# Optimization experiments

Measured on AMD Instinct MI355X. Metric: run time of the kernel, lower is better.

Reference implementation:

```python
import jax, jax.numpy as jnp
import numpy as np
from jax import lax

T, IN, H, OUT = 8192, 1, 1024, 1


def setup_inputs() -> dict:
    key = jax.random.key(0)
    ks = jax.random.split(key, 7)
    s = 1.0 / np.sqrt(H)
    return {
        "x": jax.random.normal(ks[0], (T, IN), dtype=jnp.float32),
        "W_ih": jax.random.uniform(ks[1], (4 * H, IN), jnp.float32, -s, s),
        "W_hh": jax.random.uniform(ks[2], (4 * H, H), jnp.float32, -s, s),
        "b_ih": jax.random.uniform(ks[3], (4 * H,), jnp.float32, -s, s),
        "b_hh": jax.random.uniform(ks[4], (4 * H,), jnp.float32, -s, s),
        "W_fc": jax.random.uniform(ks[5], (OUT, H), jnp.float32, -s, s),
        "b_fc": jax.random.uniform(ks[6], (OUT,), jnp.float32, -s, s),
    }


def reference(x, W_ih, W_hh, b_ih, b_hh, W_fc, b_fc):
    # x: (T, input_size); batch dim of 1 is squeezed out.
    H_ = W_hh.shape[1]
    # Precompute input contribution to all gates for every timestep: (T, 4H)
    xg = x @ W_ih.T + (b_ih + b_hh)

    def step(carry, gx):
        h, c = carry
        g = gx + h @ W_hh.T  # (4H,) -- PyTorch gate order i, f, g, o
        i, f, gg, o = jnp.split(g, 4)
        c = jax.nn.sigmoid(f) * c + jax.nn.sigmoid(i) * jnp.tanh(gg)
        h = jax.nn.sigmoid(o) * jnp.tanh(c)
        return (h, c), h

    h0 = jnp.zeros((H_,), dtype=x.dtype)
    c0 = jnp.zeros((H_,), dtype=x.dtype)
    _, hs = lax.scan(step, (h0, c0), xg)  # hs: (T, H)
    return hs @ W_fc.T + b_fc  # (T, output_size)
```

## Files before the change

### kernel.cpp

```cpp
#include <hip/hip_runtime.h>

#define TT    8192
#define HD    1024
#define NBLK  256
#define NTHR  256
#define NBUF  4
#define NREP  8

typedef int i32x4 __attribute__((ext_vector_type(4)));
typedef int i32x2 __attribute__((ext_vector_type(2)));

__device__ __forceinline__ void llc_load_pair(const unsigned* p, i32x4& a, i32x4& b) {
  asm volatile("global_load_dwordx4 %0, %2, off sc0 sc1\n\t"
               "global_load_dwordx4 %1, %3, off sc0 sc1\n\t"
               "s_waitcnt vmcnt(0)"
               : "=&v"(a), "=&v"(b)
               : "v"(p), "v"(p + 4)
               : "memory");
}
__device__ __forceinline__ unsigned llc_load1(const unsigned* p) {
  unsigned r;
  asm volatile("global_load_dword %0, %1, off sc0 sc1\n\ts_waitcnt vmcnt(0)"
               : "=v"(r) : "v"(p) : "memory");
  return r;
}
__device__ __forceinline__ void llc_store2(unsigned* p, unsigned lo, unsigned hi) {
  i32x2 v; v.x = (int)lo; v.y = (int)hi;
  asm volatile("global_store_dwordx2 %0, %1, off sc0 sc1"
               :: "v"(p), "v"(v) : "memory");
}
__device__ __forceinline__ void llc_store1(unsigned* p, unsigned v) {
  asm volatile("global_store_dword %0, %1, off sc0 sc1"
               :: "v"(p), "v"(v) : "memory");
}

__device__ __forceinline__ float sigf(float z) {
  return 1.0f / (1.0f + __expf(-z));
}
__device__ __forceinline__ float tanh_fast(float z) {
  float az = fabsf(z);
  float e  = __expf(2.0f * az);
  float t  = 1.0f - 2.0f / (e + 1.0f);
  return z < 0.0f ? -t : t;
}

#define FMA4(acc, hvv, wvv)                                      \
  acc = fmaf((hvv).x, (wvv).x, acc);                             \
  acc = fmaf((hvv).y, (wvv).y, acc);                             \
  acc = fmaf((hvv).z, (wvv).z, acc);                             \
  acc = fmaf((hvv).w, (wvv).w, acc);

extern "C" __global__ __launch_bounds__(NTHR, 1)
void lstm_persistent(const float* __restrict__ x,
                     const float* __restrict__ W_ih,
                     const float* __restrict__ W_hh,
                     const float* __restrict__ b_ih,
                     const float* __restrict__ b_hh,
                     const float* __restrict__ W_fc,
                     const float* __restrict__ b_fc,
                     float* __restrict__ out,
                     unsigned* __restrict__ flag,
                     unsigned* __restrict__ hbuf)
{
  const int tid = threadIdx.x;
  const int blk = blockIdx.x;

  if (blk == NBLK) {
    for (int t = 0; t < TT; ++t) {
      const unsigned* src = hbuf + (((t & (NBUF - 1)) * HD + tid * 4) * 2);
      i32x4 A, B;
      const int want = t + 1;
      do {
        llc_load_pair(src, A, B);
      } while (!(A.y == want && A.w == want && B.y == want && B.w == want));
      __syncthreads();
      if (tid < NREP)
        llc_store1(flag + (tid << 4), (unsigned)want);
    }
    return;
  }

  __shared__ float x_lds[TT];
  __shared__ float h_lds[HD];

  const int wave = tid >> 6;
  const int lane = tid & 63;
  const int g    = lane >> 4;
  const int kc   = lane & 15;
  const int unit = blk * 4 + wave;

  for (int i = tid; i < TT / 4; i += NTHR)
    ((float4*)x_lds)[i] = ((const float4*)x)[i];

  float4 w4[16];
  {
    const float* wr = W_hh + (size_t)(g * HD + unit) * HD + kc * 4;
#pragma unroll
    for (int m = 0; m < 16; ++m)
      w4[m] = *((const float4*)(wr + m * 64));
  }
  float4 wfc4[4];
#pragma unroll
  for (int m = 0; m < 4; ++m)
    wfc4[m] = *((const float4*)(W_fc + m * 256 + lane * 4));
  const float bfc_val = b_fc[0];

  float wih_g[4], bs_g[4];
#pragma unroll
  for (int q = 0; q < 4; ++q) {
    int r = q * HD + unit;
    wih_g[q] = W_ih[r];
    bs_g[q]  = b_ih[r] + b_hh[r];
  }
  float c_state = 0.0f;
  __syncthreads();

  const unsigned* flag_mine = flag + ((blk & (NREP - 1)) << 4);

  for (int t = 0; t < TT; ++t) {
    const bool doproj = (t > 0) && (wave == 1) && (blk == (t & 255));
    float accs = 0.0f;
    float4 hp4[4];

    if (t > 0) {
      while (llc_load1(flag_mine) < (unsigned)t) { }
      const unsigned* src = hbuf + (((t - 1) & (NBUF - 1)) * HD + tid * 4) * 2;
      i32x4 A, B;
      llc_load_pair(src, A, B);
      float4 hv;
      hv.x = __int_as_float(A.x); hv.y = __int_as_float(A.z);
      hv.z = __int_as_float(B.x); hv.w = __int_as_float(B.z);
      ((float4*)h_lds)[tid] = hv;
      __syncthreads();

      const float* hp = h_lds + kc * 4;
      float s0 = 0.f, s1 = 0.f, s2 = 0.f, s3 = 0.f;
#pragma unroll
      for (int mb = 0; mb < 4; ++mb) {
        float4 ha = *((const float4*)(hp + (mb * 4 + 0) * 64));
        float4 hb = *((const float4*)(hp + (mb * 4 + 1) * 64));
        float4 hc = *((const float4*)(hp + (mb * 4 + 2) * 64));
        float4 hd = *((const float4*)(hp + (mb * 4 + 3) * 64));
        FMA4(s0, ha, w4[mb * 4 + 0]);
        FMA4(s1, hb, w4[mb * 4 + 1]);
        FMA4(s2, hc, w4[mb * 4 + 2]);
        FMA4(s3, hd, w4[mb * 4 + 3]);
      }
      accs = (s0 + s1) + (s2 + s3);

      if (doproj) {
#pragma unroll
        for (int m = 0; m < 4; ++m)
          hp4[m] = *((const float4*)(h_lds + m * 256 + lane * 4));
      }
    }

#pragma unroll
    for (int s = 1; s < 16; s <<= 1)
      accs += __shfl_xor(accs, s);

    float gi = __shfl(accs, 0);
    float gf = __shfl(accs, 16);
    float gg = __shfl(accs, 32);
    float go = __shfl(accs, 48);

    if (lane == 0) {
      float xt = x_lds[t];
      gi += fmaf(xt, wih_g[0], bs_g[0]);
      gf += fmaf(xt, wih_g[1], bs_g[1]);
      gg += fmaf(xt, wih_g[2], bs_g[2]);
      go += fmaf(xt, wih_g[3], bs_g[3]);
      c_state  = sigf(gf) * c_state + sigf(gi) * tanh_fast(gg);
      float hn = sigf(go) * tanh_fast(c_state);
      llc_store2(hbuf + (((t & (NBUF - 1)) * HD + unit) * 2),
                 __float_as_uint(hn), (unsigned)(t + 1));
    }

    if (doproj) {
      float p = 0.f;
#pragma unroll
      for (int m = 0; m < 4; ++m) { FMA4(p, hp4[m], wfc4[m]); }
#pragma unroll
      for (int s = 1; s < 64; s <<= 1) p += __shfl_xor(p, s);
      if (lane == 0) out[t - 1] = p + bfc_val;
    }
  }

  if (blk == 0) {
    const unsigned* src = hbuf + (((TT - 1) & (NBUF - 1)) * HD + tid * 4) * 2;
    i32x4 A, B;
    do {
      llc_load_pair(src, A, B);
    } while (!(A.y == TT && A.w == TT && B.y == TT && B.w == TT));
    float4 hv;
    hv.x = __int_as_float(A.x); hv.y = __int_as_float(A.z);
    hv.z = __int_as_float(B.x); hv.w = __int_as_float(B.z);
    ((float4*)h_lds)[tid] = hv;
    __syncthreads();
    if (wave == 1) {
      float p = 0.f;
#pragma unroll
      for (int m = 0; m < 4; ++m) {
        float4 hm = *((const float4*)(h_lds + m * 256 + lane * 4));
        FMA4(p, hm, wfc4[m]);
      }
#pragma unroll
      for (int s = 1; s < 64; s <<= 1) p += __shfl_xor(p, s);
      if (lane == 0) out[TT - 1] = p + bfc_val;
    }
  }
}

extern "C" void kernel_launch(void* const* d_in, const int* in_sizes, int n_in,
                              void* d_out, int out_size, void* d_ws, size_t ws_size,
                              hipStream_t stream) {
  const float* x   = (const float*)d_in[0];
  const float* Wih = (const float*)d_in[1];
  const float* Whh = (const float*)d_in[2];
  const float* bih = (const float*)d_in[3];
  const float* bhh = (const float*)d_in[4];
  const float* Wfc = (const float*)d_in[5];
  const float* bfc = (const float*)d_in[6];
  float* out = (float*)d_out;

  unsigned* flag = (unsigned*)d_ws;
  unsigned* hbuf = flag + NREP * 16;
  size_t init_bytes = (NREP * 16 + NBUF * HD * 2) * sizeof(unsigned);

  hipMemsetAsync(d_ws, 0, init_bytes, stream);
  hipLaunchKernelGGL(lstm_persistent, dim3(NBLK + 1), dim3(NTHR), 0, stream,
                     x, Wih, Whh, bih, bhh, Wfc, bfc, out, flag, hbuf);
}
```

Baseline: 23.68 ms.

## Relay hidden state through per-XCD L2 mirror to cut cross-die polling latency

In each XCD, the first block to claim a slot through an atomic becomes a relay. Each step, the relay polls the LLC-coherent hidden-state buffer and copies it into a per-XCD mirror. The other blocks on that XCD poll the mirror with L2-scoped loads, aiming to avoid the round trip to LLC and the central flag. A bounded retry count falls back to the original flag path if the mirror stalls. The risks are plain non-coherent stores and L2 visibility ordering, plus the extra relay latency added to the critical path.

```diff
diff --git a/kernel.cpp b/kernel.cpp
--- a/kernel.cpp
+++ b/kernel.cpp
@@ -6,6 +6,8 @@
 #define NTHR  256
 #define NBUF  4
 #define NREP  8
+#define NXCD  8
+#define L2_TRIES 64
 
 typedef int i32x4 __attribute__((ext_vector_type(4)));
 typedef int i32x2 __attribute__((ext_vector_type(2)));
@@ -31,6 +33,18 @@
 }
 __device__ __forceinline__ void llc_store1(unsigned* p, unsigned v) {
   asm volatile("global_store_dword %0, %1, off sc0 sc1"
+               :: "v"(p), "v"(v) : "memory");
+}
+__device__ __forceinline__ void l2_load_pair(const unsigned* p, i32x4& a, i32x4& b) {
+  asm volatile("global_load_dwordx4 %0, %2, off sc0\n\t"
+               "global_load_dwordx4 %1, %3, off sc0\n\t"
+               "s_waitcnt vmcnt(0)"
+               : "=&v"(a), "=&v"(b)
+               : "v"(p), "v"(p + 4)
+               : "memory");
+}
+__device__ __forceinline__ void l2_store4(unsigned* p, i32x4 v) {
+  asm volatile("global_store_dwordx4 %0, %1, off"
                :: "v"(p), "v"(v) : "memory");
 }
 
@@ -59,8 +73,10 @@
                      const float* __restrict__ W_fc,
                      const float* __restrict__ b_fc,
                      float* __restrict__ out,
+                     int*      __restrict__ relay_slot,
                      unsigned* __restrict__ flag,
-                     unsigned* __restrict__ hbuf)
+                     unsigned* __restrict__ hbuf,
+                     unsigned* __restrict__ xmirror)
 {
   const int tid = threadIdx.x;
   const int blk = blockIdx.x;
@@ -72,7 +88,7 @@
       const int want = t + 1;
       do {
         llc_load_pair(src, A, B);
-      } while (!(A.y == want && A.w == want && B.y == want && B.w == want));
+      } while (!(A.y >= want && A.w >= want && B.y >= want && B.w >= want));
       __syncthreads();
       if (tid < NREP)
         llc_store1(flag + (tid << 4), (unsigned)want);
@@ -82,6 +98,7 @@
 
   __shared__ float x_lds[TT];
   __shared__ float h_lds[HD];
+  __shared__ int   info_lds[2];
 
   const int wave = tid >> 6;
   const int lane = tid & 63;
@@ -89,6 +106,15 @@
   const int kc   = lane & 15;
   const int unit = blk * 4 + wave;
 
+  if (tid == 0) {
+    int xcd;
+    asm volatile("s_getreg_b32 %0, hwreg(HW_REG_XCC_ID)" : "=s"(xcd));
+    xcd &= (NXCD - 1);
+    int old = atomicCAS(&relay_slot[xcd], -1, blk);
+    info_lds[0] = (old == -1) ? 1 : 0;
+    info_lds[1] = xcd;
+  }
+
   for (int i = tid; i < TT / 4; i += NTHR)
     ((float4*)x_lds)[i] = ((const float4*)x)[i];
 
@@ -115,7 +141,12 @@
   float c_state = 0.0f;
   __syncthreads();
 
+  const bool is_relay = (info_lds[0] != 0);
+  const int  myx      = info_lds[1];
   const unsigned* flag_mine = flag + ((blk & (NREP - 1)) << 4);
+
+  bool use_l2 = true;
+  int  l2fail = 0;
 
   for (int t = 0; t < TT; ++t) {
     const bool doproj = (t > 0) && (wave == 1) && (blk == (t & 255));
@@ -123,11 +154,37 @@
     float4 hp4[4];
 
     if (t > 0) {
-      while (llc_load1(flag_mine) < (unsigned)t) { }
-      const unsigned* src = hbuf + (((t - 1) & (NBUF - 1)) * HD + tid * 4) * 2;
+      const int slot = (t - 1) & (NBUF - 1);
+      float4 hv;
+      bool got = false;
       i32x4 A, B;
-      llc_load_pair(src, A, B);
-      float4 hv;
+
+      if (is_relay) {
+        const unsigned* src = hbuf + ((size_t)slot * HD + tid * 4) * 2;
+        do {
+          llc_load_pair(src, A, B);
+        } while (!(A.y == t && A.w == t && B.y == t && B.w == t));
+        unsigned* dst = xmirror + (((size_t)myx * NBUF + slot) * HD + tid * 4) * 2;
+        l2_store4(dst, A);
+        l2_store4(dst + 4, B);
+        got = true;
+      } else {
+        if (use_l2) {
+          const unsigned* msrc =
+              xmirror + (((size_t)myx * NBUF + slot) * HD + tid * 4) * 2;
+          for (int it = 0; it < L2_TRIES; ++it) {
+            l2_load_pair(msrc, A, B);
+            if (A.y == t && A.w == t && B.y == t && B.w == t) { got = true; break; }
+          }
+          if (got) l2fail = 0;
+          else if (++l2fail >= 2) use_l2 = false;
+        }
+        if (!got) {
+          while (llc_load1(flag_mine) < (unsigned)t) { }
+          const unsigned* src = hbuf + ((size_t)slot * HD + tid * 4) * 2;
+          llc_load_pair(src, A, B);
+        }
+      }
       hv.x = __int_as_float(A.x); hv.y = __int_as_float(A.z);
       hv.z = __int_as_float(B.x); hv.w = __int_as_float(B.z);
       ((float4*)h_lds)[tid] = hv;
@@ -223,11 +280,16 @@
   const float* bfc = (const float*)d_in[6];
   float* out = (float*)d_out;
 
-  unsigned* flag = (unsigned*)d_ws;
-  unsigned* hbuf = flag + NREP * 16;
-  size_t init_bytes = (NREP * 16 + NBUF * HD * 2) * sizeof(unsigned);
-
-  hipMemsetAsync(d_ws, 0, init_bytes, stream);
+  char* base = (char*)d_ws;
+  int*      relay_slot = (int*)base;
+  unsigned* flag    = (unsigned*)(base + 256);
+  unsigned* hbuf    = (unsigned*)(base + 768);
+  unsigned* xmirror = (unsigned*)(base + 768 + NBUF * HD * 2 * sizeof(unsigned));
+  size_t zero_bytes = 512 + (NBUF * HD * 2 + NXCD * NBUF * HD * 2) * sizeof(unsigned);
+
+  hipMemsetAsync(base, 0xFF, 256, stream);
+  hipMemsetAsync(base + 256, 0, zero_bytes, stream);
   hipLaunchKernelGGL(lstm_persistent, dim3(NBLK + 1), dim3(NTHR), 0, stream,
-                     x, Wih, Whh, bih, bhh, Wfc, bfc, out, flag, hbuf);
-}
+                     x, Wih, Whh, bih, bhh, Wfc, bfc, out,
+                     relay_slot, flag, hbuf, xmirror);
+}
```

Result: slower. 62.13 ms (+162.4%).
